# Optimization experiments

Hardware: AMD Instinct MI355X
Metric: run time of the kernel (lower is better)

Reference implementation:

```python
import jax, jax.numpy as jnp
import numpy as np

D = 128      # input_dim (= out_channels = edge_dim)
H = 2        # n_head
N_ENT = 100000
B = 64       # number of queries / batches
R = 500      # number of relations
E = 400000   # number of original edges
NEG = 0.2    # GATv2 leaky_relu negative slope


def setup_inputs() -> dict:
    key = jax.random.key(0)
    ks = jax.random.split(key, 10)
    s = 1.0 / np.sqrt(D)
    queries = jax.random.normal(ks[0], (B, D), jnp.float32)
    entities = jax.random.normal(ks[1], (N_ENT, D), jnp.float32)
    edge_index = jax.random.randint(ks[2], (2, E), 0, N_ENT)
    relations = jax.random.normal(ks[3], (R, D), jnp.float32)
    relation_index = jax.random.randint(ks[4], (E,), 0, R)
    # guarantees batch.max()+1 == queries.shape[0] (module assert)
    batch = jnp.arange(N_ENT, dtype=jnp.int32) % B
    # GATv2Conv params: lin_l / lin_r (bias=True), lin_edge (bias=False), att, bias
    W_l = jax.random.normal(ks[5], (H * D, D), jnp.float32) * s
    b_l = jnp.zeros((H * D,), jnp.float32)
    W_r = jax.random.normal(ks[6], (H * D, D), jnp.float32) * s
    b_r = jnp.zeros((H * D,), jnp.float32)
    W_ea = jax.random.normal(ks[7], (H * D, D), jnp.float32) * s
    att = jax.random.normal(ks[8], (H, D), jnp.float32) * s
    bias = jnp.zeros((D,), jnp.float32)  # concat=False -> size out_channels
    # outer Injector.lin_edge: Linear(H*D, D, bias=True)
    W_le = jax.random.normal(ks[9], (D, H * D), jnp.float32) / np.sqrt(H * D)
    b_le = jnp.zeros((D,), jnp.float32)
    return dict(queries=queries, entities=entities, edge_index=edge_index,
                relations=relations, relation_index=relation_index, batch=batch,
                W_l=W_l, b_l=b_l, W_r=W_r, b_r=b_r, W_ea=W_ea, att=att,
                bias=bias, W_le=W_le, b_le=b_le)


def reference(queries, entities, edge_index, relations, relation_index, batch,
              W_l, b_l, W_r, b_r, W_ea, att, bias, W_le, b_le):
    n_ent = entities.shape[0]
    node = jnp.vstack([entities, queries])                        # [N+B, D]
    rel_feat = jnp.vstack([relations,
                           jnp.ones((1, relations.shape[1]), relations.dtype)])
    # added edges: query -> its entities
    src = jnp.concatenate([edge_index[0], batch.astype(edge_index.dtype) + n_ent])
    tgt = jnp.concatenate([edge_index[1],
                           jnp.arange(n_ent, dtype=edge_index.dtype)])
    rel_idx = jnp.concatenate([relation_index,
                               jnp.full((n_ent,), rel_feat.shape[0] - 1,
                                        relation_index.dtype)])
    edge_attr = rel_feat[rel_idx]                                  # [Etot, D]

    n_tot = node.shape[0]
    x_l = (node @ W_l.T + b_l).reshape(n_tot, H, D)                # source proj
    x_r = (node @ W_r.T + b_r).reshape(n_tot, H, D)                # target proj
    e = (edge_attr @ W_ea.T).reshape(-1, H, D)                     # [Etot, H, D]

    xj = x_l[src]                                                  # gather per edge
    z = jax.nn.leaky_relu(xj + x_r[tgt] + e, NEG)                  # [Etot, H, D]
    alpha = jnp.einsum('ehd,hd->eh', z, att)                       # [Etot, H]
    # segment softmax over target nodes
    amax = jax.ops.segment_max(alpha, tgt, num_segments=n_tot)
    alpha = jnp.exp(alpha - amax[tgt])
    denom = jax.ops.segment_sum(alpha, tgt, num_segments=n_tot)
    alpha = alpha / (denom[tgt] + 1e-16)

    msg = xj * alpha[..., None]                                    # [Etot, H, D]
    agg = jax.ops.segment_sum(msg, tgt, num_segments=n_tot)        # [Ntot, H, D]
    out = agg.mean(axis=1) + bias                                  # concat=False
    out_node = out[:n_ent]

    out_edge = jax.nn.relu(relations @ W_ea.T)                     # [R, H*D]
    out_edge = out_edge @ W_le.T + b_le                            # [R, D]
    return (out_node, out_edge)
```

## Files before the change

kernel.cpp:

```cpp
#include <hip/hip_runtime.h>
#include <math.h>

#define D 128
#define HD 256
#define N_ENT 100000
#define NBATCH 64
#define NTOT (N_ENT + NBATCH)
#define RCOUNT 500
#define E_BASE 400000
#define ETOT (E_BASE + N_ENT)
#define NEG 0.2f
#define SCAN_NB 391
#define CPAD (SCAN_NB * 256)

#define WCAST_NB 64
#define ZERO_NB SCAN_NB
#define REL_NB (RCOUNT + 1)
#define PREP_NB (WCAST_NB + ZERO_NB + REL_NB)

#define GEMM_NB ((NTOT + 63) / 64)
#define HIST_NB ((ETOT + 255) / 256)
#define EDGE_NB 6250

typedef __attribute__((ext_vector_type(8))) short bf16x8;
typedef __attribute__((ext_vector_type(8))) unsigned short u16x8;
typedef __attribute__((ext_vector_type(4))) float f32x4;
typedef __attribute__((ext_vector_type(2))) float f32x2;

static __device__ __forceinline__ unsigned short f2bf(float f) {
  unsigned u = __builtin_bit_cast(unsigned, f);
  u += 0x7fffu + ((u >> 16) & 1u);
  return (unsigned short)(u >> 16);
}
static __device__ __forceinline__ float bf2f(unsigned short h) {
  return __builtin_bit_cast(float, (unsigned)h << 16);
}
static __device__ __forceinline__ f32x2 bfpair(unsigned u) {
  f32x2 r;
  r[0] = __builtin_bit_cast(float, u << 16);
  r[1] = __builtin_bit_cast(float, u & 0xffff0000u);
  return r;
}

static __device__ __forceinline__ float dpp_red16(float p) {
  int t;
  t = __builtin_amdgcn_update_dpp(0, __builtin_bit_cast(int, p), 0xB1, 0xF, 0xF, true);
  p += __builtin_bit_cast(float, t);
  t = __builtin_amdgcn_update_dpp(0, __builtin_bit_cast(int, p), 0x4E, 0xF, 0xF, true);
  p += __builtin_bit_cast(float, t);
  t = __builtin_amdgcn_update_dpp(0, __builtin_bit_cast(int, p), 0x141, 0xF, 0xF, true);
  p += __builtin_bit_cast(float, t);
  t = __builtin_amdgcn_update_dpp(0, __builtin_bit_cast(int, p), 0x140, 0xF, 0xF, true);
  p += __builtin_bit_cast(float, t);
  return p;
}

__global__ __launch_bounds__(256) void k_prep(
    const float* __restrict__ W_l, const float* __restrict__ W_r,
    unsigned short* __restrict__ Wbf,
    const float* __restrict__ relations, const float* __restrict__ W_ea,
    const float* __restrict__ W_le, const float* __restrict__ b_le,
    unsigned short* __restrict__ e_rel, float* __restrict__ out_edge,
    int* __restrict__ counts) {
  __shared__ float relu_p[HD];
  int bx = blockIdx.x;
  int tid = threadIdx.x;
  if (bx < WCAST_NB) {
    int e4 = (bx * 256 + tid) * 4;
    int v = e4 >> 7;
    int k = e4 & 127;
    const float* src = (v < HD) ? (W_l + (size_t)v * D + k) : (W_r + (size_t)(v - HD) * D + k);
    float4 a = *(const float4*)src;
    *(ushort4*)(Wbf + (size_t)v * D + k) = make_ushort4(f2bf(a.x), f2bf(a.y), f2bf(a.z), f2bf(a.w));
    return;
  }
  if (bx < WCAST_NB + ZERO_NB) {
    counts[(bx - WCAST_NB) * 256 + tid] = 0;
    return;
  }
  int r = bx - (WCAST_NB + ZERO_NB);
  int j = tid;
  const float* w = W_ea + (size_t)j * D;
  float acc = 0.f;
  if (r < RCOUNT) {
    const float* rel = relations + (size_t)r * D;
    for (int k = 0; k < D; k += 4) {
      float4 a = *(const float4*)(rel + k);
      float4 b = *(const float4*)(w + k);
      acc += a.x * b.x + a.y * b.y + a.z * b.z + a.w * b.w;
    }
  } else {
    for (int k = 0; k < D; k += 4) {
      float4 b = *(const float4*)(w + k);
      acc += b.x + b.y + b.z + b.w;
    }
  }
  e_rel[(size_t)r * HD + j] = f2bf(acc);
  if (r < RCOUNT) {
    relu_p[j] = acc > 0.f ? acc : 0.f;
    __syncthreads();
    if (j < D) {
      const float* wl = W_le + (size_t)j * HD;
      float o = b_le[j];
      for (int k = 0; k < HD; k += 4) {
        float4 p4 = *(const float4*)(relu_p + k);
        float4 w4 = *(const float4*)(wl + k);
        o += p4.x * w4.x + p4.y * w4.y + p4.z * w4.z + p4.w * w4.w;
      }
      out_edge[(size_t)r * D + j] = o;
    }
  }
}

#define LDA 136

__global__ __launch_bounds__(256) void k_gemm_mfma(
    const float* __restrict__ entities, const float* __restrict__ queries,
    const unsigned short* __restrict__ Wbf,
    const float* __restrict__ b_l, const float* __restrict__ b_r,
    unsigned short* __restrict__ x_l, unsigned short* __restrict__ x_r,
    const int* __restrict__ edge_index, int* __restrict__ counts) {
  __shared__ unsigned short As[64 * LDA];
  __shared__ unsigned short Cs[64 * LDA];
  int tid = threadIdx.x;
  if (blockIdx.x >= GEMM_NB) {
    int e = (blockIdx.x - GEMM_NB) * 256 + tid;
    if (e < ETOT) {
      int t = (e < E_BASE) ? edge_index[E_BASE + e] : (e - E_BASE);
      atomicAdd(counts + t, 1);
    }
    return;
  }
  int rb = blockIdx.x;

  {
    int rr = tid >> 2;
    int part = (tid & 3) * 32;
    int row = rb * 64 + rr;
    const float* sp;
    if (row < N_ENT) sp = entities + (size_t)row * D;
    else if (row < NTOT) sp = queries + (size_t)(row - N_ENT) * D;
    else sp = entities;
#pragma unroll
    for (int k = 0; k < 32; k += 8) {
      float4 a0 = *(const float4*)(sp + part + k);
      float4 a1 = *(const float4*)(sp + part + k + 4);
      u16x8 p;
      p[0] = f2bf(a0.x); p[1] = f2bf(a0.y); p[2] = f2bf(a0.z); p[3] = f2bf(a0.w);
      p[4] = f2bf(a1.x); p[5] = f2bf(a1.y); p[6] = f2bf(a1.z); p[7] = f2bf(a1.w);
      *(u16x8*)(&As[rr * LDA + part + k]) = p;
    }
  }
  __syncthreads();

  int w = tid >> 6, lane = tid & 63;
  int wr = w >> 1, wc = w & 1;
  int m = lane & 15, q8 = (lane >> 4) * 8;

  for (int ccv = 0; ccv < 4; ccv++) {
    bool isL = ccv < 2;
    const float* bv = isL ? b_l : b_r;
    unsigned short* xdst = isL ? x_l : x_r;
    int cbase = (ccv & 1) * 128;

    f32x4 acc[2][4];
#pragma unroll
    for (int i = 0; i < 2; i++)
#pragma unroll
      for (int j = 0; j < 4; j++) acc[i][j] = (f32x4){0.f, 0.f, 0.f, 0.f};

    const unsigned short* wbase = Wbf + (size_t)(ccv * 128 + wc * 64 + m) * D;
#pragma unroll
    for (int ks = 0; ks < 128; ks += 32) {
      bf16x8 af[2], bfr[4];
#pragma unroll
      for (int i = 0; i < 2; i++)
        af[i] = *(const bf16x8*)(&As[(wr * 32 + i * 16 + m) * LDA + ks + q8]);
#pragma unroll
      for (int j = 0; j < 4; j++)
        bfr[j] = *(const bf16x8*)(wbase + (size_t)j * 16 * D + ks + q8);
#pragma unroll
      for (int i = 0; i < 2; i++)
#pragma unroll
        for (int j = 0; j < 4; j++)
          acc[i][j] = __builtin_amdgcn_mfma_f32_16x16x32_bf16(af[i], bfr[j], acc[i][j], 0, 0, 0);
    }

    __syncthreads();
#pragma unroll
    for (int j = 0; j < 4; j++) {
      int col = wc * 64 + j * 16 + m;
      float bb = bv[cbase + col];
#pragma unroll
      for (int i = 0; i < 2; i++) {
        int row0 = wr * 32 + i * 16 + (lane >> 4) * 4;
#pragma unroll
        for (int r = 0; r < 4; r++)
          Cs[(row0 + r) * LDA + col] = f2bf(acc[i][j][r] + bb);
      }
    }
    __syncthreads();
#pragma unroll
    for (int it = 0; it < 4; it++) {
      int g = it * 256 + tid;
      int row = g >> 4, c8 = (g & 15) * 8;
      int grow = rb * 64 + row;
      if (grow < NTOT) {
        u16x8 v = *(const u16x8*)(&Cs[row * LDA + c8]);
        *(u16x8*)(xdst + (size_t)grow * HD + cbase + c8) = v;
      }
    }
  }
}

__global__ __launch_bounds__(256) void k_scan_a(const int* __restrict__ counts, int* __restrict__ bsum) {
  __shared__ int sd[256];
  int tid = threadIdx.x;
  sd[tid] = counts[blockIdx.x * 256 + tid];
  __syncthreads();
  for (int off = 128; off > 0; off >>= 1) {
    if (tid < off) sd[tid] += sd[tid + off];
    __syncthreads();
  }
  if (tid == 0) bsum[blockIdx.x] = sd[0];
}

__global__ __launch_bounds__(256) void k_scan_b(
    const int* __restrict__ counts, const int* __restrict__ bsum,
    int* __restrict__ offsets, int* __restrict__ cursor) {
  __shared__ int s[256];
  int b = blockIdx.x, tid = threadIdx.x;
  int part = 0;
  if (tid < b) part += bsum[tid];
  if (tid + 256 < b) part += bsum[tid + 256];
  s[tid] = part;
  __syncthreads();
  for (int off = 128; off > 0; off >>= 1) {
    if (tid < off) s[tid] += s[tid + off];
    __syncthreads();
  }
  int pre_sum = s[0];
  __syncthreads();
  int v = counts[b * 256 + tid];
  s[tid] = v;
  __syncthreads();
  for (int off = 1; off < 256; off <<= 1) {
    int y = (tid >= off) ? s[tid - off] : 0;
    __syncthreads();
    s[tid] += y;
    __syncthreads();
  }
  int excl = pre_sum + s[tid] - v;
  int i = b * 256 + tid;
  if (i <= N_ENT) offsets[i] = excl;
  if (i < N_ENT) cursor[i] = excl;
}

__global__ void k_scatter(const int* __restrict__ edge_index, const int* __restrict__ relation_index,
                          const int* __restrict__ batch, int* __restrict__ cursor,
                          unsigned* __restrict__ sorted) {
  int e = blockIdx.x * 256 + threadIdx.x;
  if (e >= ETOT) return;
  int s, t, r;
  if (e < E_BASE) {
    s = edge_index[e];
    t = edge_index[E_BASE + e];
    r = relation_index[e];
  } else {
    int i = e - E_BASE;
    s = N_ENT + batch[i];
    t = i;
    r = RCOUNT;
  }
  int pos = atomicAdd(cursor + t, 1);
  sorted[pos] = (unsigned)s | ((unsigned)r << 17);
}

static __device__ __forceinline__ float edge_accum(
    u16x8 xl8, u16x8 er8, const f32x2* __restrict__ xr2,
    const f32x2* __restrict__ at2, f32x2* __restrict__ x2) {
  uint4 xu = __builtin_bit_cast(uint4, xl8);
  uint4 eu = __builtin_bit_cast(uint4, er8);
  unsigned xw[4] = {xu.x, xu.y, xu.z, xu.w};
  unsigned ew[4] = {eu.x, eu.y, eu.z, eu.w};
  f32x2 p2 = (f32x2){0.f, 0.f};
#pragma unroll
  for (int i = 0; i < 4; ++i) {
    f32x2 x = bfpair(xw[i]);
    x2[i] = x;
    f32x2 z = (x + xr2[i]) + bfpair(ew[i]);
    f32x2 zn = z * NEG;
    z[0] = fmaxf(z[0], zn[0]);
    z[1] = fmaxf(z[1], zn[1]);
    p2 += z * at2[i];
  }
  return p2[0] + p2[1];
}

__global__ __launch_bounds__(256) void k_edge(
    const unsigned short* __restrict__ x_l, const unsigned short* __restrict__ x_r,
    const unsigned short* __restrict__ e_rel, const int* __restrict__ offsets,
    const unsigned* __restrict__ sorted, const float* __restrict__ att,
    const float* __restrict__ bias, float* __restrict__ out) {
  int wv = threadIdx.x >> 6;
  int lane = threadIdx.x & 63;
  int half = lane >> 5;
  int sl = lane & 31;
  int elem = sl * 8;
  int t0 = (blockIdx.x * 4 + wv) * 4;

  const char* xlb = (const char*)x_l + elem * 2;
  const char* erb = (const char*)e_rel + elem * 2;

  f32x2 at2[4];
  {
    float4 a0 = *(const float4*)(att + elem);
    float4 a1 = *(const float4*)(att + elem + 4);
    at2[0] = (f32x2){a0.x, a0.y};
    at2[1] = (f32x2){a0.z, a0.w};
    at2[2] = (f32x2){a1.x, a1.y};
    at2[3] = (f32x2){a1.z, a1.w};
  }
  int4 ofs = *(const int4*)(offsets + t0);
  int eb[5];
  eb[0] = ofs.x; eb[1] = ofs.y; eb[2] = ofs.z; eb[3] = ofs.w;
  eb[4] = offsets[t0 + 4];

  u16x8 xr8 = __builtin_nontemporal_load((const u16x8*)(x_r + (size_t)t0 * HD + elem));

#pragma unroll
  for (int ti = 0; ti < 4; ++ti) {
    f32x2 xr2[4];
    {
      uint4 u = __builtin_bit_cast(uint4, xr8);
      xr2[0] = bfpair(u.x); xr2[1] = bfpair(u.y);
      xr2[2] = bfpair(u.z); xr2[3] = bfpair(u.w);
    }
    xr8 = __builtin_nontemporal_load((const u16x8*)(x_r + (size_t)(t0 + ti + 1) * HD + elem));

    int e0 = eb[ti], e1 = eb[ti + 1];
    f32x2 acc2[4];
    acc2[0] = acc2[1] = acc2[2] = acc2[3] = (f32x2){0.f, 0.f};
    float denom = 0.f;
    int e = e0;
    for (; e + 4 <= e1; e += 4) {
      unsigned srA = sorted[e + half];
      unsigned srB = sorted[e + 2 + half];
      u16x8 xlA = *(const u16x8*)(xlb + ((size_t)(srA & 0x1FFFFu) << 9));
      u16x8 erA = *(const u16x8*)(erb + ((size_t)(srA >> 17) << 9));
      u16x8 xlB = *(const u16x8*)(xlb + ((size_t)(srB & 0x1FFFFu) << 9));
      u16x8 erB = *(const u16x8*)(erb + ((size_t)(srB >> 17) << 9));
      f32x2 xa2[4], xb2[4];
      float pa = edge_accum(xlA, erA, xr2, at2, xa2);
      float pb = edge_accum(xlB, erB, xr2, at2, xb2);
      pa = dpp_red16(pa);
      pb = dpp_red16(pb);
      float wa = __expf(pa);
      float wb = __expf(pb);
      denom += wa + wb;
#pragma unroll
      for (int i = 0; i < 4; ++i) {
        acc2[i] += xa2[i] * wa;
        acc2[i] += xb2[i] * wb;
      }
    }
    for (; e < e1; e += 2) {
      int ee = e + half;
      bool valid = ee < e1;
      unsigned sr = sorted[valid ? ee : e0];
      u16x8 xl8 = *(const u16x8*)(xlb + ((size_t)(sr & 0x1FFFFu) << 9));
      u16x8 er8 = *(const u16x8*)(erb + ((size_t)(sr >> 17) << 9));
      f32x2 x2[4];
      float p = edge_accum(xl8, er8, xr2, at2, x2);
      p = dpp_red16(p);
      float wgt = valid ? __expf(p) : 0.f;
      denom += wgt;
#pragma unroll
      for (int i = 0; i < 4; ++i) acc2[i] += x2[i] * wgt;
    }
    denom += __shfl_xor(denom, 32, 64);
#pragma unroll
    for (int i = 0; i < 4; ++i) {
      acc2[i][0] += __shfl_xor(acc2[i][0], 32, 64);
      acc2[i][1] += __shfl_xor(acc2[i][1], 32, 64);
    }
    float inv = 0.5f / (denom + 1e-16f);
    float o[8];
#pragma unroll
    for (int i = 0; i < 4; ++i) {
      o[2 * i] = acc2[i][0] * inv;
      o[2 * i + 1] = acc2[i][1] * inv;
    }
#pragma unroll
    for (int i = 0; i < 8; ++i) o[i] += __shfl_xor(o[i], 16, 64);
    if (lane < 16) {
      int t = t0 + ti;
      int d = sl * 8;
      float4 b0 = *(const float4*)(bias + d);
      float4 b1 = *(const float4*)(bias + d + 4);
      f32x4 s0 = (f32x4){o[0] + b0.x, o[1] + b0.y, o[2] + b0.z, o[3] + b0.w};
      f32x4 s1 = (f32x4){o[4] + b1.x, o[5] + b1.y, o[6] + b1.z, o[7] + b1.w};
      __builtin_nontemporal_store(s0, (f32x4*)(out + (size_t)t * D + d));
      __builtin_nontemporal_store(s1, (f32x4*)(out + (size_t)t * D + d + 4));
    }
  }
}

extern "C" void kernel_launch(void* const* d_in, const int* in_sizes, int n_in,
                              void* d_out, int out_size, void* d_ws, size_t ws_size,
                              hipStream_t stream) {
  const float* queries = (const float*)d_in[0];
  const float* entities = (const float*)d_in[1];
  const int* edge_index = (const int*)d_in[2];
  const float* relations = (const float*)d_in[3];
  const int* relation_index = (const int*)d_in[4];
  const int* batch = (const int*)d_in[5];
  const float* W_l = (const float*)d_in[6];
  const float* b_l = (const float*)d_in[7];
  const float* W_r = (const float*)d_in[8];
  const float* b_r = (const float*)d_in[9];
  const float* W_ea = (const float*)d_in[10];
  const float* att = (const float*)d_in[11];
  const float* bias = (const float*)d_in[12];
  const float* W_le = (const float*)d_in[13];
  const float* b_le = (const float*)d_in[14];

  float* out_node = (float*)d_out;
  float* out_edge = out_node + (size_t)N_ENT * D;

  char* base = (char*)d_ws;
  size_t off = 0;
  auto take = [&](size_t nbytes) -> void* {
    void* p = base + off;
    off += (nbytes + 255) & ~(size_t)255;
    return p;
  };
  unsigned short* x_l = (unsigned short*)take((size_t)NTOT * HD * sizeof(unsigned short));
  unsigned short* x_r = (unsigned short*)take((size_t)NTOT * HD * sizeof(unsigned short));
  unsigned short* e_rel = (unsigned short*)take((size_t)(RCOUNT + 1) * HD * sizeof(unsigned short));
  unsigned short* Wbf = (unsigned short*)take((size_t)512 * D * sizeof(unsigned short));
  int* counts = (int*)take((size_t)CPAD * sizeof(int));
  int* offsets = (int*)take((size_t)(N_ENT + 1) * sizeof(int));
  int* cursor = (int*)take((size_t)N_ENT * sizeof(int));
  int* bsum = (int*)take(512 * sizeof(int));
  unsigned* sorted = (unsigned*)take((size_t)ETOT * sizeof(unsigned));

  k_prep<<<dim3(PREP_NB), dim3(256), 0, stream>>>(W_l, W_r, Wbf, relations, W_ea, W_le, b_le,
                                                  e_rel, out_edge, counts);
  k_gemm_mfma<<<dim3(GEMM_NB + HIST_NB), dim3(256), 0, stream>>>(entities, queries, Wbf, b_l, b_r,
                                                                 x_l, x_r, edge_index, counts);
  k_scan_a<<<dim3(SCAN_NB), dim3(256), 0, stream>>>(counts, bsum);
  k_scan_b<<<dim3(SCAN_NB), dim3(256), 0, stream>>>(counts, bsum, offsets, cursor);
  k_scatter<<<dim3(HIST_NB), dim3(256), 0, stream>>>(edge_index, relation_index, batch, cursor, sorted);
  k_edge<<<dim3(EDGE_NB), dim3(256), 0, stream>>>(x_l, x_r, e_rel, offsets, sorted, att, bias, out_node);
}
```

Before: 296.6 us.

## Record histogram ranks to drop scatter atomics, use hardware bf16 convert, widen edge tiles

The histogram pass now stores each edge's atomicAdd return value as its rank. The scatter kernel then computes its position as offsets[t] + rank[e] and no longer needs a cursor array with a second round of atomics. Software bf16 rounding is replaced with the v_cvt_pk_bf16_f32 instruction for packed conversion. The edge kernel now handles 8 targets per wave instead of 4, halving the grid size. The cost is an extra rank buffer of one int per edge, and fewer blocks in the edge kernel may reduce occupancy and latency hiding.

```diff
diff --git a/kernel.cpp b/kernel.cpp
--- a/kernel.cpp
+++ b/kernel.cpp
@@ -20,20 +20,23 @@
 
 #define GEMM_NB ((NTOT + 63) / 64)
 #define HIST_NB ((ETOT + 255) / 256)
-#define EDGE_NB 6250
+#define EDGE_TPW 8
+#define EDGE_NB (N_ENT / (4 * EDGE_TPW))
 
 typedef __attribute__((ext_vector_type(8))) short bf16x8;
 typedef __attribute__((ext_vector_type(8))) unsigned short u16x8;
 typedef __attribute__((ext_vector_type(4))) float f32x4;
 typedef __attribute__((ext_vector_type(2))) float f32x2;
 
-static __device__ __forceinline__ unsigned short f2bf(float f) {
-  unsigned u = __builtin_bit_cast(unsigned, f);
-  u += 0x7fffu + ((u >> 16) & 1u);
-  return (unsigned short)(u >> 16);
-}
-static __device__ __forceinline__ float bf2f(unsigned short h) {
-  return __builtin_bit_cast(float, (unsigned)h << 16);
+static __device__ __forceinline__ unsigned cvt_pk_bf16(float lo, float hi) {
+  unsigned r;
+  asm("v_cvt_pk_bf16_f32 %0, %1, %2" : "=v"(r) : "v"(lo), "v"(hi));
+  return r;
+}
+static __device__ __forceinline__ unsigned short f2bf_hw(float f) {
+  unsigned r;
+  asm("v_cvt_pk_bf16_f32 %0, %1, %1" : "=v"(r) : "v"(f));
+  return (unsigned short)r;
 }
 static __device__ __forceinline__ f32x2 bfpair(unsigned u) {
   f32x2 r;
@@ -71,7 +74,10 @@
     int k = e4 & 127;
     const float* src = (v < HD) ? (W_l + (size_t)v * D + k) : (W_r + (size_t)(v - HD) * D + k);
     float4 a = *(const float4*)src;
-    *(ushort4*)(Wbf + (size_t)v * D + k) = make_ushort4(f2bf(a.x), f2bf(a.y), f2bf(a.z), f2bf(a.w));
+    uint2 p;
+    p.x = cvt_pk_bf16(a.x, a.y);
+    p.y = cvt_pk_bf16(a.z, a.w);
+    *(uint2*)(Wbf + (size_t)v * D + k) = p;
     return;
   }
   if (bx < WCAST_NB + ZERO_NB) {
@@ -95,7 +101,7 @@
       acc += b.x + b.y + b.z + b.w;
     }
   }
-  e_rel[(size_t)r * HD + j] = f2bf(acc);
+  e_rel[(size_t)r * HD + j] = f2bf_hw(acc);
   if (r < RCOUNT) {
     relu_p[j] = acc > 0.f ? acc : 0.f;
     __syncthreads();
@@ -119,7 +125,8 @@
     const unsigned short* __restrict__ Wbf,
     const float* __restrict__ b_l, const float* __restrict__ b_r,
     unsigned short* __restrict__ x_l, unsigned short* __restrict__ x_r,
-    const int* __restrict__ edge_index, int* __restrict__ counts) {
+    const int* __restrict__ edge_index, int* __restrict__ counts,
+    int* __restrict__ rank) {
   __shared__ unsigned short As[64 * LDA];
   __shared__ unsigned short Cs[64 * LDA];
   int tid = threadIdx.x;
@@ -127,7 +134,7 @@
     int e = (blockIdx.x - GEMM_NB) * 256 + tid;
     if (e < ETOT) {
       int t = (e < E_BASE) ? edge_index[E_BASE + e] : (e - E_BASE);
-      atomicAdd(counts + t, 1);
+      rank[e] = atomicAdd(counts + t, 1);
     }
     return;
   }
@@ -145,10 +152,12 @@
     for (int k = 0; k < 32; k += 8) {
       float4 a0 = *(const float4*)(sp + part + k);
       float4 a1 = *(const float4*)(sp + part + k + 4);
-      u16x8 p;
-      p[0] = f2bf(a0.x); p[1] = f2bf(a0.y); p[2] = f2bf(a0.z); p[3] = f2bf(a0.w);
-      p[4] = f2bf(a1.x); p[5] = f2bf(a1.y); p[6] = f2bf(a1.z); p[7] = f2bf(a1.w);
-      *(u16x8*)(&As[rr * LDA + part + k]) = p;
+      uint4 p;
+      p.x = cvt_pk_bf16(a0.x, a0.y);
+      p.y = cvt_pk_bf16(a0.z, a0.w);
+      p.z = cvt_pk_bf16(a1.x, a1.y);
+      p.w = cvt_pk_bf16(a1.z, a1.w);
+      *(uint4*)(&As[rr * LDA + part + k]) = p;
     }
   }
   __syncthreads();
@@ -196,7 +205,7 @@
         int row0 = wr * 32 + i * 16 + (lane >> 4) * 4;
 #pragma unroll
         for (int r = 0; r < 4; r++)
-          Cs[(row0 + r) * LDA + col] = f2bf(acc[i][j][r] + bb);
+          Cs[(row0 + r) * LDA + col] = f2bf_hw(acc[i][j][r] + bb);
       }
     }
     __syncthreads();
@@ -227,7 +236,7 @@
 
 __global__ __launch_bounds__(256) void k_scan_b(
     const int* __restrict__ counts, const int* __restrict__ bsum,
-    int* __restrict__ offsets, int* __restrict__ cursor) {
+    int* __restrict__ offsets) {
   __shared__ int s[256];
   int b = blockIdx.x, tid = threadIdx.x;
   int part = 0;
@@ -253,12 +262,11 @@
   int excl = pre_sum + s[tid] - v;
   int i = b * 256 + tid;
   if (i <= N_ENT) offsets[i] = excl;
-  if (i < N_ENT) cursor[i] = excl;
 }
 
 __global__ void k_scatter(const int* __restrict__ edge_index, const int* __restrict__ relation_index,
-                          const int* __restrict__ batch, int* __restrict__ cursor,
-                          unsigned* __restrict__ sorted) {
+                          const int* __restrict__ batch, const int* __restrict__ offsets,
+                          const int* __restrict__ rank, unsigned* __restrict__ sorted) {
   int e = blockIdx.x * 256 + threadIdx.x;
   if (e >= ETOT) return;
   int s, t, r;
@@ -272,7 +280,7 @@
     t = i;
     r = RCOUNT;
   }
-  int pos = atomicAdd(cursor + t, 1);
+  int pos = offsets[t] + rank[e];
   sorted[pos] = (unsigned)s | ((unsigned)r << 17);
 }
 
@@ -307,7 +315,7 @@
   int half = lane >> 5;
   int sl = lane & 31;
   int elem = sl * 8;
-  int t0 = (blockIdx.x * 4 + wv) * 4;
+  int t0 = (blockIdx.x * 4 + wv) * EDGE_TPW;
 
   const char* xlb = (const char*)x_l + elem * 2;
   const char* erb = (const char*)e_rel + elem * 2;
@@ -321,15 +329,19 @@
     at2[2] = (f32x2){a1.x, a1.y};
     at2[3] = (f32x2){a1.z, a1.w};
   }
-  int4 ofs = *(const int4*)(offsets + t0);
-  int eb[5];
-  eb[0] = ofs.x; eb[1] = ofs.y; eb[2] = ofs.z; eb[3] = ofs.w;
-  eb[4] = offsets[t0 + 4];
+  int eb[EDGE_TPW + 1];
+  {
+    int4 o0 = *(const int4*)(offsets + t0);
+    int4 o1 = *(const int4*)(offsets + t0 + 4);
+    eb[0] = o0.x; eb[1] = o0.y; eb[2] = o0.z; eb[3] = o0.w;
+    eb[4] = o1.x; eb[5] = o1.y; eb[6] = o1.z; eb[7] = o1.w;
+    eb[8] = offsets[t0 + 8];
+  }
 
   u16x8 xr8 = __builtin_nontemporal_load((const u16x8*)(x_r + (size_t)t0 * HD + elem));
 
 #pragma unroll
-  for (int ti = 0; ti < 4; ++ti) {
+  for (int ti = 0; ti < EDGE_TPW; ++ti) {
     f32x2 xr2[4];
     {
       uint4 u = __builtin_bit_cast(uint4, xr8);
@@ -441,16 +453,16 @@
   unsigned short* Wbf = (unsigned short*)take((size_t)512 * D * sizeof(unsigned short));
   int* counts = (int*)take((size_t)CPAD * sizeof(int));
   int* offsets = (int*)take((size_t)(N_ENT + 1) * sizeof(int));
-  int* cursor = (int*)take((size_t)N_ENT * sizeof(int));
+  int* rank = (int*)take((size_t)ETOT * sizeof(int));
   int* bsum = (int*)take(512 * sizeof(int));
   unsigned* sorted = (unsigned*)take((size_t)ETOT * sizeof(unsigned));
 
   k_prep<<<dim3(PREP_NB), dim3(256), 0, stream>>>(W_l, W_r, Wbf, relations, W_ea, W_le, b_le,
                                                   e_rel, out_edge, counts);
   k_gemm_mfma<<<dim3(GEMM_NB + HIST_NB), dim3(256), 0, stream>>>(entities, queries, Wbf, b_l, b_r,
-                                                                 x_l, x_r, edge_index, counts);
+                                                                 x_l, x_r, edge_index, counts, rank);
   k_scan_a<<<dim3(SCAN_NB), dim3(256), 0, stream>>>(counts, bsum);
-  k_scan_b<<<dim3(SCAN_NB), dim3(256), 0, stream>>>(counts, bsum, offsets, cursor);
-  k_scatter<<<dim3(HIST_NB), dim3(256), 0, stream>>>(edge_index, relation_index, batch, cursor, sorted);
+  k_scan_b<<<dim3(SCAN_NB), dim3(256), 0, stream>>>(counts, bsum, offsets);
+  k_scatter<<<dim3(HIST_NB), dim3(256), 0, stream>>>(edge_index, relation_index, batch, offsets, rank, sorted);
   k_edge<<<dim3(EDGE_NB), dim3(256), 0, stream>>>(x_l, x_r, e_rel, offsets, sorted, att, bias, out_node);
 }
```

Result: faster. 286.2 us (-3.5%).
